# Optimization experiments

Measured on AMD Instinct MI355X. Metric: run time of the kernel, lower is better.

## Reference

```python
import jax, jax.numpy as jnp
import numpy as np

N = 512       # num_nodes (feature dim of x == num_nodes, per GCNConv(num_nodes, f1))
BZ = 32       # subjects
TC = 256      # tc_length
F1 = 256
F2 = 128
E = 524288    # edges in the given (corr) graph over all bz*N nodes
NTOT = BZ * N
SLOPE = 0.2   # leaky relu negative_slope


def setup_inputs() -> dict:
    key = jax.random.key(0)
    ks = jax.random.split(key, 17)
    w = lambda k, shape: (jax.random.normal(k, shape, jnp.float32) * (shape[-1] ** -0.5))
    return {
        "x": jax.random.normal(ks[0], (NTOT, N), jnp.float32),
        "t": jax.random.normal(ks[1], (NTOT, TC), jnp.float32),
        "gumbel_u": jax.random.uniform(ks[2], (BZ, N, N, 2), jnp.float32),
        "edge_index": jax.random.randint(ks[3], (2, E), 0, NTOT, jnp.int64 if jax.config.jax_enable_x64 else jnp.int32),
        "conv1_w": w(ks[4], (F1, N)),
        "conv1_b": jnp.zeros((F1,), jnp.float32),
        "conv2_w": w(ks[5], (F2, F1)),
        "conv2_b": jnp.zeros((F2,), jnp.float32),
        "fc_cat_w": w(ks[6], (2, 2 * TC)),
        "fc_cat_b": jnp.zeros((2,), jnp.float32),
        "fcn1_w": w(ks[7], (256, F2 * 2 * N)),
        "fcn1_b": jnp.zeros((256,), jnp.float32),
        "fcn2_w": w(ks[8], (32, 256)),
        "fcn2_b": jnp.zeros((32,), jnp.float32),
        "fcn3_w": w(ks[9], (2, 32)),
        "fcn3_b": jnp.zeros((2,), jnp.float32),
    }


def _gcn_dense(x, A, W, b):
    # PyG GCNConv on a dense 0/1 adjacency A (edge r->c means A[r,c]=1):
    # add self loop, in-degree symmetric norm, aggregate sources into targets.
    n = A.shape[0]
    Ah = A + jnp.eye(n, dtype=A.dtype)
    deg = Ah.sum(axis=0)                                  # in-degree (targets = cols)
    dis = jnp.where(deg > 0, jax.lax.rsqrt(deg), 0.0)
    M = dis[:, None] * Ah * dis[None, :]                  # M[j,i] = d_j^-1/2 A_hat[j,i] d_i^-1/2
    return M.T @ (x @ W.T) + b


def _gcn_sparse(x, row, col, W, b):
    n = x.shape[0]
    loops = jnp.arange(n, dtype=row.dtype)
    r = jnp.concatenate([row, loops])
    c = jnp.concatenate([col, loops])
    deg = jax.ops.segment_sum(jnp.ones_like(c, x.dtype), c, num_segments=n)
    dis = jnp.where(deg > 0, jax.lax.rsqrt(deg), 0.0)
    norm = dis[r] * dis[c]                                # [E+n]
    xw = x @ W.T                                          # [n, out]
    out = jax.ops.segment_sum(xw[r] * norm[:, None], c, num_segments=n)
    return out + b


def reference(x, t, gumbel_u, edge_index, conv1_w, conv1_b, conv2_w, conv2_b,
              fc_cat_w, fc_cat_b, fcn1_w, fcn1_b, fcn2_w, fcn2_b, fcn3_w, fcn3_b):
    bz = t.shape[0] // N
    tb = t.reshape(bz, N, -1)
    xb = x.reshape(bz, N, -1)
    # fc_cat(relu(cat([senders, receivers]))) factors into per-node terms:
    Ws = fc_cat_w[:, :TC]   # multiplies senders half
    Wr = fc_cat_w[:, TC:]   # multiplies receivers half

    def per_sample(ti, xi, ui):
        u = jax.nn.relu(ti)                               # [N, TC]
        ls = u @ Ws.T                                     # [N, 2] sender term
        lr = u @ Wr.T                                     # [N, 2] receiver term
        # pair k = i*N+j has receiver t_i, sender t_j
        logits = lr[:, None, :] + ls[None, :, :] + fc_cat_b   # [N, N, 2]
        g = -jnp.log(-jnp.log(jnp.clip(ui, 1e-9, 1.0 - 1e-9)))  # Gumbel(0,1)
        y = logits + g                                    # tau = 1
        A = (jnp.argmax(y, axis=-1) == 0).astype(xi.dtype)    # hard sample, class 0 => edge
        A = jax.lax.stop_gradient(A)                      # torch.where -> indices blocks grad
        h = jax.nn.relu(_gcn_dense(xi, A, conv1_w, conv1_b))
        return _gcn_dense(h, A, conv2_w, conv2_b)         # [N, F2]

    x_op = jax.vmap(per_sample)(tb, xb, gumbel_u)         # [bz, N, F2]

    row, col = edge_index[0], edge_index[1]
    x_corr = jax.nn.relu(_gcn_sparse(x, row, col, conv1_w, conv1_b))
    x_corr = _gcn_sparse(x_corr, row, col, conv2_w, conv2_b)   # [bz*N, F2]

    emb = jnp.concatenate([x_op.reshape(-1, F2), x_corr], axis=1)  # [bz*N, 2*F2]
    emb = emb.reshape(bz, -1)                             # [bz, 2*F2*N]
    h = jax.nn.leaky_relu(emb @ fcn1_w.T + fcn1_b, SLOPE)
    h = jax.nn.leaky_relu(h @ fcn2_w.T + fcn2_b, SLOPE)
    return h @ fcn3_w.T + fcn3_b                          # [bz, 2]
```

## Files before the change

kernel.cpp:

```cpp
#include <hip/hip_runtime.h>
#include <hip/hip_bf16.h>

typedef __bf16 bf16_t;
typedef __bf16 bf16x8 __attribute__((ext_vector_type(8)));
typedef __bf16 bf16x4 __attribute__((ext_vector_type(4)));
typedef float f32x4 __attribute__((ext_vector_type(4)));

constexpr int kN = 512;
constexpr int kBZ = 32;
constexpr int kTC = 256;
constexpr int kE = 524288;
constexpr int kNTOT = 16384;

__global__ __launch_bounds__(256) void k_cvt3(const float* __restrict__ c1w, const float* __restrict__ c2w,
                                              bf16_t* __restrict__ c1b, bf16_t* __restrict__ c2b,
                                              int* __restrict__ counts, float* __restrict__ degsum) {
    int i = blockIdx.x * 256 + threadIdx.x;
    const int n0 = 32768, n1 = n0 + 8192, n2 = n1 + 4096, n3 = n2 + 4096;
    if (i < n0) {
        float4 v = ((const float4*)c1w)[i];
        bf16x4 o = {(bf16_t)v.x, (bf16_t)v.y, (bf16_t)v.z, (bf16_t)v.w};
        ((bf16x4*)c1b)[i] = o;
    } else if (i < n1) {
        int j = i - n0;
        float4 v = ((const float4*)c2w)[j];
        bf16x4 o = {(bf16_t)v.x, (bf16_t)v.y, (bf16_t)v.z, (bf16_t)v.w};
        ((bf16x4*)c2b)[j] = o;
    } else if (i < n2) {
        ((int4*)counts)[i - n1] = make_int4(0, 0, 0, 0);
    } else if (i < n3) {
        ((float4*)degsum)[i - n2] = make_float4(0.f, 0.f, 0.f, 0.f);
    }
}

__global__ __launch_bounds__(256) void k_lsr(const float* __restrict__ tin, const float* __restrict__ fcw,
                                             const float* __restrict__ fcb, float4* __restrict__ lsr) {
    int row = blockIdx.x * 4 + (threadIdx.x >> 6);
    int lane = threadIdx.x & 63;
    const float* tr = tin + (size_t)row * kTC;
    float s0 = 0, s1 = 0, r0 = 0, r1 = 0;
    for (int k = lane; k < kTC; k += 64) {
        float u = fmaxf(tr[k], 0.f);
        s0 += u * fcw[k];
        s1 += u * fcw[512 + k];
        r0 += u * fcw[256 + k];
        r1 += u * fcw[768 + k];
    }
#pragma unroll
    for (int off = 32; off > 0; off >>= 1) {
        s0 += __shfl_down(s0, off); s1 += __shfl_down(s1, off);
        r0 += __shfl_down(r0, off); r1 += __shfl_down(r1, off);
    }
    if (lane == 0) lsr[row] = make_float4(s0 + fcb[0], s1 + fcb[1], r0, r1);
}

__global__ __launch_bounds__(256) void k_adj(const float* __restrict__ gum, const float4* __restrict__ lsr,
                                             bf16_t* __restrict__ AT, float* __restrict__ degsum) {
    int s = blockIdx.z;
    int a0 = blockIdx.y * 64, b0 = blockIdx.x * 64;
    __shared__ bf16_t tile[64][72];
    int t = threadIdx.x;
    int lb = t & 63, ra = t >> 6;
    int b = b0 + lb;
    float4 pb = lsr[s * kN + b];
#pragma unroll 4
    for (int p = 0; p < 16; p++) {
        int a = a0 + p * 4 + ra;
        float4 qa = lsr[s * kN + a];
        const float* g = gum + ((((size_t)s * kN + a) * kN + b) << 1);
        float u0 = fmaxf(g[0], 1e-9f);
        float u1 = fmaxf(g[1], 1e-9f);
        float g0 = -__logf(-__logf(u0));
        float g1 = -__logf(-__logf(u1));
        float v = ((qa.z + pb.x + g0) >= (qa.w + pb.y + g1)) ? 1.f : 0.f;
        if (a == b) v += 1.f;
        tile[lb][p * 4 + ra] = (bf16_t)v;
    }
    __syncthreads();
    int rj = t >> 3, li = (t & 7) * 8;
#pragma unroll
    for (int p = 0; p < 2; p++) {
        int j = p * 32 + rj;
        bf16x8 v = *(const bf16x8*)&tile[j][li];
        *(bf16x8*)(AT + ((size_t)s * kN + b0 + j) * kN + a0 + li) = v;
        float ps = 0;
#pragma unroll
        for (int q = 0; q < 8; q++) ps += (float)v[q];
        ps += __shfl_down(ps, 4);
        ps += __shfl_down(ps, 2);
        ps += __shfl_down(ps, 1);
        if ((t & 7) == 0) atomicAdd(degsum + s * kN + b0 + j, ps);
    }
}

template <int MODE>
__global__ __launch_bounds__(256) void k_gemm(const bf16_t* __restrict__ A, const bf16_t* __restrict__ B,
                                              bf16_t* __restrict__ C, int K, int lda, int ldb, int ldc,
                                              size_t sA, size_t sB, size_t sC,
                                              const float* __restrict__ degsum, const float* __restrict__ bias) {
    int m0 = blockIdx.x * 128, n0 = blockIdx.y * 128, s = blockIdx.z;
    A += sA * s; B += sB * s; C += sC * s;
    __shared__ bf16_t As[128][72], Bs[128][72];
    f32x4 acc[4][4] = {};
    int tid = threadIdx.x;
    int wave = tid >> 6, lane = tid & 63;
    int wm = (wave & 1) * 64, wn = (wave >> 1) * 64;
    int fm = lane & 15, fq = lane >> 4;
    int srow = tid >> 3, scol = (tid & 7) * 8;
    for (int kb = 0; kb < K; kb += 64) {
        __syncthreads();
#pragma unroll
        for (int p = 0; p < 4; p++) {
            int row = p * 32 + srow;
            *(uint4*)&As[row][scol] = *(const uint4*)(A + (size_t)(m0 + row) * lda + kb + scol);
            *(uint4*)&Bs[row][scol] = *(const uint4*)(B + (size_t)(n0 + row) * ldb + kb + scol);
        }
        __syncthreads();
#pragma unroll
        for (int kk = 0; kk < 2; kk++) {
            bf16x8 af[4], bfr[4];
#pragma unroll
            for (int i = 0; i < 4; i++) {
                af[i] = *(const bf16x8*)&As[wm + i * 16 + fm][kk * 32 + fq * 8];
                bfr[i] = *(const bf16x8*)&Bs[wn + i * 16 + fm][kk * 32 + fq * 8];
            }
#pragma unroll
            for (int i = 0; i < 4; i++)
#pragma unroll
                for (int j = 0; j < 4; j++)
                    acc[i][j] = __builtin_amdgcn_mfma_f32_16x16x32_bf16(af[i], bfr[j], acc[i][j], 0, 0, 0);
        }
    }
#pragma unroll
    for (int i = 0; i < 4; i++) {
#pragma unroll
        for (int r = 0; r < 4; r++) {
            int row = wm + i * 16 + fq * 4 + r;
            float sc = rsqrtf(degsum[(size_t)s * kN + m0 + row]);
#pragma unroll
            for (int j = 0; j < 4; j++) {
                int col = n0 + wn + j * 16 + fm;
                float v = sc * acc[i][j][r] + bias[col];
                if constexpr (MODE == 1) v = fmaxf(v, 0.f);
                C[(size_t)(m0 + row) * ldc + col] = (bf16_t)v;
            }
        }
    }
}

template <bool AF32, int F, int DENSE_ROWS>
__global__ __launch_bounds__(256) void k_gemmT(const void* __restrict__ Ap, const bf16_t* __restrict__ B,
                                               bf16_t* __restrict__ XW, bf16_t* __restrict__ ZT, int K,
                                               const float* __restrict__ degsum) {
    int m0 = blockIdx.x * 128, n0 = blockIdx.y * 128;
    __shared__ __align__(16) bf16_t smem[2 * 128 * 72];
    bf16_t* AsBase = smem;
    bf16_t* BsBase = smem + 128 * 72;
    f32x4 acc[4][4] = {};
    int tid = threadIdx.x;
    int wave = tid >> 6, lane = tid & 63;
    int wm = (wave & 1) * 64, wn = (wave >> 1) * 64;
    int fm = lane & 15, fq = lane >> 4;
    int srow = tid >> 3, scol = (tid & 7) * 8;
    for (int kb = 0; kb < K; kb += 64) {
        __syncthreads();
#pragma unroll
        for (int p = 0; p < 4; p++) {
            int row = p * 32 + srow;
            if constexpr (AF32) {
                const float* ap = (const float*)Ap + (size_t)(m0 + row) * K + kb + scol;
                float4 lo = *(const float4*)ap;
                float4 hi = *(const float4*)(ap + 4);
                bf16x8 o = {(bf16_t)lo.x, (bf16_t)lo.y, (bf16_t)lo.z, (bf16_t)lo.w,
                            (bf16_t)hi.x, (bf16_t)hi.y, (bf16_t)hi.z, (bf16_t)hi.w};
                *(bf16x8*)&AsBase[row * 72 + scol] = o;
            } else {
                *(uint4*)&AsBase[row * 72 + scol] =
                    *(const uint4*)((const bf16_t*)Ap + (size_t)(m0 + row) * K + kb + scol);
            }
            *(uint4*)&BsBase[row * 72 + scol] = *(const uint4*)(B + (size_t)(n0 + row) * K + kb + scol);
        }
        __syncthreads();
#pragma unroll
        for (int kk = 0; kk < 2; kk++) {
            bf16x8 af[4], bfr[4];
#pragma unroll
            for (int i = 0; i < 4; i++) {
                af[i] = *(const bf16x8*)&AsBase[(wm + i * 16 + fm) * 72 + kk * 32 + fq * 8];
                bfr[i] = *(const bf16x8*)&BsBase[(wn + i * 16 + fm) * 72 + kk * 32 + fq * 8];
            }
#pragma unroll
            for (int i = 0; i < 4; i++)
#pragma unroll
                for (int j = 0; j < 4; j++)
                    acc[i][j] = __builtin_amdgcn_mfma_f32_16x16x32_bf16(af[i], bfr[j], acc[i][j], 0, 0, 0);
        }
    }
    bool doT = (m0 < DENSE_ROWS);
    __syncthreads();
#pragma unroll
    for (int i = 0; i < 4; i++) {
#pragma unroll
        for (int r = 0; r < 4; r++) {
            int row = wm + i * 16 + fq * 4 + r;
            float sc = doT ? rsqrtf(degsum[m0 + row]) : 0.f;
#pragma unroll
            for (int j = 0; j < 4; j++) {
                int col = wn + j * 16 + fm;
                float v = acc[i][j][r];
                XW[(size_t)(m0 + row) * F + n0 + col] = (bf16_t)v;
                if (doT) smem[col * 136 + row] = (bf16_t)(sc * v);
            }
        }
    }
    if (doT) {
        __syncthreads();
        int fr = tid >> 1, hi = (tid & 1) * 64;
        bf16_t* zrow = ZT + ((size_t)(m0 >> 9) * F + n0 + fr) * kN + (m0 & 511) + hi;
#pragma unroll
        for (int q = 0; q < 8; q++)
            *(bf16x8*)(zrow + q * 8) = *(const bf16x8*)&smem[fr * 136 + hi + q * 8];
    }
}


__global__ __launch_bounds__(256) void k_hist(const int* __restrict__ col, int* __restrict__ counts) {
    int e = blockIdx.x * 256 + threadIdx.x;
    if (e < kE) atomicAdd(&counts[col[e]], 1);
}

__global__ __launch_bounds__(256) void k_scan(const int* __restrict__ counts, int* __restrict__ offsets,
                                              int* __restrict__ cursor, float* __restrict__ dis_s) {
    __shared__ int ldc_[16896];
    __shared__ int sums[256];
    int t = threadIdx.x;
#define IDX(j) ((j) + ((j) >> 5))
    for (int i = 0; i < 64; i++) {
        int g = i * 256 + t;
        int c = counts[g];
        ldc_[IDX(g)] = c;
        dis_s[g] = rsqrtf((float)(c + 1));
    }
    __syncthreads();
    int s = 0;
    for (int i = 0; i < 64; i++) s += ldc_[IDX(t * 64 + i)];
    sums[t] = s;
    __syncthreads();
    for (int off = 1; off < 256; off <<= 1) {
        int y = (t >= off) ? sums[t - off] : 0;
        __syncthreads();
        sums[t] += y;
        __syncthreads();
    }
    int run = sums[t] - s;
    for (int i = 0; i < 64; i++) {
        int j = t * 64 + i;
        int c = ldc_[IDX(j)];
        ldc_[IDX(j)] = run;
        run += c;
    }
    __syncthreads();
    for (int i = 0; i < 64; i++) {
        int g = i * 256 + t;
        int o = ldc_[IDX(g)];
        offsets[g] = o;
        cursor[g] = o;
    }
#undef IDX
}

__global__ __launch_bounds__(256) void k_fill(const int* __restrict__ row, const int* __restrict__ col,
                                              int* __restrict__ cursor, int* __restrict__ list) {
    int e = blockIdx.x * 256 + threadIdx.x;
    if (e < kE) {
        int p = atomicAdd(&cursor[col[e]], 1);
        list[p] = row[e];
    }
}

template <int F, bool RELU>
__global__ __launch_bounds__(256) void k_sagg(const bf16_t* __restrict__ XW, int rowOffIn,
                                              const int* __restrict__ list, const int* __restrict__ offsets,
                                              const int* __restrict__ counts, const float* __restrict__ dis_s,
                                              const float* __restrict__ bias, bf16_t* __restrict__ OUT,
                                              int outColOff) {
    constexpr int TPR = F / 8;
    constexpr int RPB = 256 / TPR;
    int j = blockIdx.x * RPB + threadIdx.x / TPR;
    int f8 = (threadIdx.x % TPR) * 8;
    float dj = dis_s[j];
    const bf16_t* base = XW + (size_t)rowOffIn * F;
    float acc[8];
    {
        bf16x8 v = *(const bf16x8*)(base + (size_t)j * F + f8);
#pragma unroll
        for (int q = 0; q < 8; q++) acc[q] = dj * (float)v[q];
    }
    int off = offsets[j], cnt = counts[j];
    int e = 0;
    for (; e + 4 <= cnt; e += 4) {
        int r0 = list[off + e], r1 = list[off + e + 1], r2 = list[off + e + 2], r3 = list[off + e + 3];
        float d0 = dis_s[r0], d1 = dis_s[r1], d2 = dis_s[r2], d3 = dis_s[r3];
        bf16x8 v0 = *(const bf16x8*)(base + (size_t)r0 * F + f8);
        bf16x8 v1 = *(const bf16x8*)(base + (size_t)r1 * F + f8);
        bf16x8 v2 = *(const bf16x8*)(base + (size_t)r2 * F + f8);
        bf16x8 v3 = *(const bf16x8*)(base + (size_t)r3 * F + f8);
#pragma unroll
        for (int q = 0; q < 8; q++)
            acc[q] += (d0 * (float)v0[q] + d1 * (float)v1[q]) + (d2 * (float)v2[q] + d3 * (float)v3[q]);
    }
    for (; e < cnt; e++) {
        int r = list[off + e];
        float d = dis_s[r];
        bf16x8 v = *(const bf16x8*)(base + (size_t)r * F + f8);
#pragma unroll
        for (int q = 0; q < 8; q++) acc[q] += d * (float)v[q];
    }
    bf16x8 o;
#pragma unroll
    for (int q = 0; q < 8; q++) {
        float v = dj * acc[q] + bias[f8 + q];
        if (RELU) v = fmaxf(v, 0.f);
        o[q] = (bf16_t)v;
    }
    *(bf16x8*)(OUT + (size_t)j * 256 + outColOff + f8) = o;
}

__global__ __launch_bounds__(256) void k_fcn1(const bf16_t* __restrict__ EMB, const float* __restrict__ W1,
                                              float* __restrict__ partials) {
    int tid = threadIdx.x, wave = tid >> 6, lane = tid & 63;
    int fm = lane & 15, fq = lane >> 4;
    int kb0 = blockIdx.x * 128;
    f32x4 acc[2][4] = {};
#pragma unroll
    for (int ks = 0; ks < 128; ks += 32) {
        int k = kb0 + ks + fq * 8;
        bf16x8 a0 = *(const bf16x8*)(EMB + (size_t)fm * 131072 + k);
        bf16x8 a1 = *(const bf16x8*)(EMB + (size_t)(16 + fm) * 131072 + k);
        bf16x8 bfr[4];
#pragma unroll
        for (int j = 0; j < 4; j++) {
            int n = wave * 64 + j * 16 + fm;
            const float* p = W1 + (size_t)n * 131072 + k;
            float4 lo = *(const float4*)p;
            float4 hi = *(const float4*)(p + 4);
            bf16x8 b = {(bf16_t)lo.x, (bf16_t)lo.y, (bf16_t)lo.z, (bf16_t)lo.w,
                        (bf16_t)hi.x, (bf16_t)hi.y, (bf16_t)hi.z, (bf16_t)hi.w};
            bfr[j] = b;
        }
#pragma unroll
        for (int j = 0; j < 4; j++) {
            acc[0][j] = __builtin_amdgcn_mfma_f32_16x16x32_bf16(a0, bfr[j], acc[0][j], 0, 0, 0);
            acc[1][j] = __builtin_amdgcn_mfma_f32_16x16x32_bf16(a1, bfr[j], acc[1][j], 0, 0, 0);
        }
    }
    float* P = partials + (size_t)blockIdx.x * 8192;
#pragma unroll
    for (int i = 0; i < 2; i++)
#pragma unroll
        for (int j = 0; j < 4; j++)
#pragma unroll
            for (int r = 0; r < 4; r++)
                P[(size_t)(i * 16 + fq * 4 + r) * 256 + wave * 64 + j * 16 + fm] = acc[i][j][r];
}

__global__ __launch_bounds__(256) void k_reduce(const float* __restrict__ partials, float* __restrict__ part2) {
    int kg = blockIdx.x >> 5, eb = blockIdx.x & 31;
    int e = eb * 256 + threadIdx.x;
    float s = 0;
#pragma unroll 8
    for (int i = 0; i < 128; i++) s += partials[(size_t)(kg * 128 + i) * 8192 + e];
    part2[(size_t)kg * 8192 + e] = s;
}

__global__ __launch_bounds__(256) void k_head(const float* __restrict__ part2, const float* __restrict__ b1,
                                              const float* __restrict__ W2, const float* __restrict__ b2,
                                              const float* __restrict__ W3, const float* __restrict__ b3,
                                              float* __restrict__ out) {
    __shared__ float h1s[32][256];
    __shared__ float h2s[32][32];
    int t = threadIdx.x;
    for (int i = 0; i < 32; i++) {
        int e = i * 256 + t;
        float s = 0;
#pragma unroll
        for (int kg = 0; kg < 8; kg++) s += part2[kg * 8192 + e];
        s += b1[t];
        h1s[i][t] = (s > 0.f) ? s : 0.2f * s;
    }
    __syncthreads();
    for (int p = 0; p < 4; p++) {
        int id = p * 256 + t, si = id >> 5, o2 = id & 31;
        float s = 0;
        for (int k = 0; k < 256; k++) s += h1s[si][k] * W2[o2 * 256 + k];
        s += b2[o2];
        h2s[si][o2] = (s > 0.f) ? s : 0.2f * s;
    }
    __syncthreads();
    if (t < 64) {
        int si = t >> 1, o3 = t & 1;
        float s = 0;
#pragma unroll
        for (int k = 0; k < 32; k++) s += h2s[si][k] * W3[o3 * 32 + k];
        out[si * 2 + o3] = s + b3[o3];
    }
}


extern "C" void kernel_launch(void* const* d_in, const int* in_sizes, int n_in,
                              void* d_out, int out_size, void* d_ws, size_t ws_size,
                              hipStream_t stream) {
    const float* x = (const float*)d_in[0];
    const float* t = (const float*)d_in[1];
    const float* gum = (const float*)d_in[2];
    const int* eidx = (const int*)d_in[3];
    const float* c1w = (const float*)d_in[4];
    const float* c1b = (const float*)d_in[5];
    const float* c2w = (const float*)d_in[6];
    const float* c2b = (const float*)d_in[7];
    const float* fcw = (const float*)d_in[8];
    const float* fcb = (const float*)d_in[9];
    const float* w1 = (const float*)d_in[10];
    const float* b1 = (const float*)d_in[11];
    const float* w2 = (const float*)d_in[12];
    const float* b2 = (const float*)d_in[13];
    const float* w3 = (const float*)d_in[14];
    const float* b3 = (const float*)d_in[15];
    float* out = (float*)d_out;
    (void)in_sizes; (void)n_in; (void)out_size; (void)ws_size;

    char* ws = (char*)d_ws;
    size_t off = 0;
    auto alloc = [&](size_t bytes) -> char* {
        char* p = ws + off;
        off += (bytes + 255) & ~size_t(255);
        return p;
    };
    bf16_t* c1wb = (bf16_t*)alloc((size_t)256 * 512 * 2);
    bf16_t* c2wb = (bf16_t*)alloc((size_t)128 * 256 * 2);
    float4* lsr = (float4*)alloc((size_t)kNTOT * 16);
    bf16_t* AT = (bf16_t*)alloc((size_t)kBZ * kN * kN * 2);
    float* degsum = (float*)alloc((size_t)kNTOT * 4);
    bf16_t* XW1_EMB = (bf16_t*)alloc((size_t)kNTOT * 256 * 2);
    bf16_t* Z1T = (bf16_t*)alloc((size_t)kBZ * 256 * 512 * 2);
    bf16_t* H = (bf16_t*)alloc((size_t)32768 * 256 * 2);
    bf16_t* XW2 = (bf16_t*)alloc((size_t)32768 * 128 * 2);
    bf16_t* Z2T = (bf16_t*)alloc((size_t)kBZ * 128 * 512 * 2);
    int* counts = (int*)alloc((size_t)kNTOT * 4);
    int* offsets = (int*)alloc((size_t)kNTOT * 4);
    int* cursor = (int*)alloc((size_t)kNTOT * 4);
    float* diss = (float*)alloc((size_t)kNTOT * 4);
    int* list = (int*)alloc((size_t)kE * 4);
    float* partials = (float*)alloc((size_t)1024 * 8192 * 4);
    float* part2 = (float*)alloc((size_t)8 * 8192 * 4);

    bf16_t* XW1 = XW1_EMB;
    bf16_t* EMB = XW1_EMB;

    k_cvt3<<<192, 256, 0, stream>>>(c1w, c2w, c1wb, c2wb, counts, degsum);
    k_lsr<<<4096, 256, 0, stream>>>(t, fcw, fcb, lsr);
    k_adj<<<dim3(8, 8, 32), 256, 0, stream>>>(gum, lsr, AT, degsum);
    k_hist<<<2048, 256, 0, stream>>>(eidx + kE, counts);
    k_scan<<<1, 256, 0, stream>>>(counts, offsets, cursor, diss);
    k_fill<<<2048, 256, 0, stream>>>(eidx, eidx + kE, cursor, list);
    k_gemmT<true, 256, kNTOT><<<dim3(128, 2, 1), 256, 0, stream>>>(x, c1wb, XW1, Z1T, 512, degsum);
    k_gemm<1><<<dim3(4, 2, 32), 256, 0, stream>>>(AT, Z1T, H, 512, 512, 512, 256,
                                                  (size_t)512 * 512, (size_t)256 * 512, (size_t)512 * 256,
                                                  degsum, c1b);
    k_sagg<256, true><<<2048, 256, 0, stream>>>(XW1, 0, list, offsets, counts, diss, c1b,
                                                H + (size_t)16384 * 256, 0);
    k_gemmT<false, 128, kNTOT><<<dim3(256, 1, 1), 256, 0, stream>>>(H, c2wb, XW2, Z2T, 256, degsum);
    k_gemm<2><<<dim3(4, 1, 32), 256, 0, stream>>>(AT, Z2T, EMB, 512, 512, 512, 256,
                                                  (size_t)512 * 512, (size_t)128 * 512, (size_t)512 * 256,
                                                  degsum, c2b);
    k_sagg<128, false><<<1024, 256, 0, stream>>>(XW2, 16384, list, offsets, counts, diss, c2b, EMB, 128);
    k_fcn1<<<1024, 256, 0, stream>>>(EMB, w1, partials);
    k_reduce<<<256, 256, 0, stream>>>(partials, part2);
    k_head<<<1, 256, 0, stream>>>(part2, b1, w2, b2, w3, b3, out);
}
```

Before: 517.2 us.

## Merge front kernels, widen scan, unroll sparse gather, and coarsen fcn1 split-K

Merges the weight-conversion/zeroing kernel and the lsr projection kernel into one launch. The single-block scan now runs 1024 threads instead of 256. The Gumbel noise pair is read as one float2 load, and the sparse aggregation gains an 8-way unrolled edge loop for more loads in flight. fcn1 now gives each block 512 K values instead of 128, so there are 256 partials rather than 1024, and the reduction becomes one pass over 256 partials. The aim is fewer launches and less partial-sum traffic, at the cost of less parallelism in fcn1 and in the reduction.

```diff
diff --git a/kernel.cpp b/kernel.cpp
--- a/kernel.cpp
+++ b/kernel.cpp
@@ -12,46 +12,51 @@
 constexpr int kE = 524288;
 constexpr int kNTOT = 16384;
 
-__global__ __launch_bounds__(256) void k_cvt3(const float* __restrict__ c1w, const float* __restrict__ c2w,
-                                              bf16_t* __restrict__ c1b, bf16_t* __restrict__ c2b,
-                                              int* __restrict__ counts, float* __restrict__ degsum) {
-    int i = blockIdx.x * 256 + threadIdx.x;
-    const int n0 = 32768, n1 = n0 + 8192, n2 = n1 + 4096, n3 = n2 + 4096;
-    if (i < n0) {
-        float4 v = ((const float4*)c1w)[i];
-        bf16x4 o = {(bf16_t)v.x, (bf16_t)v.y, (bf16_t)v.z, (bf16_t)v.w};
-        ((bf16x4*)c1b)[i] = o;
-    } else if (i < n1) {
-        int j = i - n0;
-        float4 v = ((const float4*)c2w)[j];
-        bf16x4 o = {(bf16_t)v.x, (bf16_t)v.y, (bf16_t)v.z, (bf16_t)v.w};
-        ((bf16x4*)c2b)[j] = o;
-    } else if (i < n2) {
-        ((int4*)counts)[i - n1] = make_int4(0, 0, 0, 0);
-    } else if (i < n3) {
-        ((float4*)degsum)[i - n2] = make_float4(0.f, 0.f, 0.f, 0.f);
-    }
-}
-
-__global__ __launch_bounds__(256) void k_lsr(const float* __restrict__ tin, const float* __restrict__ fcw,
-                                             const float* __restrict__ fcb, float4* __restrict__ lsr) {
-    int row = blockIdx.x * 4 + (threadIdx.x >> 6);
-    int lane = threadIdx.x & 63;
-    const float* tr = tin + (size_t)row * kTC;
-    float s0 = 0, s1 = 0, r0 = 0, r1 = 0;
-    for (int k = lane; k < kTC; k += 64) {
-        float u = fmaxf(tr[k], 0.f);
-        s0 += u * fcw[k];
-        s1 += u * fcw[512 + k];
-        r0 += u * fcw[256 + k];
-        r1 += u * fcw[768 + k];
-    }
-#pragma unroll
-    for (int off = 32; off > 0; off >>= 1) {
-        s0 += __shfl_down(s0, off); s1 += __shfl_down(s1, off);
-        r0 += __shfl_down(r0, off); r1 += __shfl_down(r1, off);
-    }
-    if (lane == 0) lsr[row] = make_float4(s0 + fcb[0], s1 + fcb[1], r0, r1);
+__global__ __launch_bounds__(256) void k_front(const float* __restrict__ c1w, const float* __restrict__ c2w,
+                                               bf16_t* __restrict__ c1b, bf16_t* __restrict__ c2b,
+                                               int* __restrict__ counts, float* __restrict__ degsum,
+                                               float* __restrict__ h1acc,
+                                               const float* __restrict__ tin, const float* __restrict__ fcw,
+                                               const float* __restrict__ fcb, float4* __restrict__ lsr) {
+    int b = blockIdx.x;
+    if (b < 200) {
+        int i = b * 256 + threadIdx.x;
+        const int n0 = 32768, n1 = n0 + 8192, n2 = n1 + 4096, n3 = n2 + 4096, n4 = n3 + 2048;
+        if (i < n0) {
+            float4 v = ((const float4*)c1w)[i];
+            bf16x4 o = {(bf16_t)v.x, (bf16_t)v.y, (bf16_t)v.z, (bf16_t)v.w};
+            ((bf16x4*)c1b)[i] = o;
+        } else if (i < n1) {
+            int j = i - n0;
+            float4 v = ((const float4*)c2w)[j];
+            bf16x4 o = {(bf16_t)v.x, (bf16_t)v.y, (bf16_t)v.z, (bf16_t)v.w};
+            ((bf16x4*)c2b)[j] = o;
+        } else if (i < n2) {
+            ((int4*)counts)[i - n1] = make_int4(0, 0, 0, 0);
+        } else if (i < n3) {
+            ((float4*)degsum)[i - n2] = make_float4(0.f, 0.f, 0.f, 0.f);
+        } else if (i < n4) {
+            ((float4*)h1acc)[i - n3] = make_float4(0.f, 0.f, 0.f, 0.f);
+        }
+    } else {
+        int row = (b - 200) * 4 + (threadIdx.x >> 6);
+        int lane = threadIdx.x & 63;
+        const float* tr = tin + (size_t)row * kTC;
+        float s0 = 0, s1 = 0, r0 = 0, r1 = 0;
+        for (int k = lane; k < kTC; k += 64) {
+            float u = fmaxf(tr[k], 0.f);
+            s0 += u * fcw[k];
+            s1 += u * fcw[512 + k];
+            r0 += u * fcw[256 + k];
+            r1 += u * fcw[768 + k];
+        }
+#pragma unroll
+        for (int off = 32; off > 0; off >>= 1) {
+            s0 += __shfl_down(s0, off); s1 += __shfl_down(s1, off);
+            r0 += __shfl_down(r0, off); r1 += __shfl_down(r1, off);
+        }
+        if (lane == 0) lsr[row] = make_float4(s0 + fcb[0], s1 + fcb[1], r0, r1);
+    }
 }
 
 __global__ __launch_bounds__(256) void k_adj(const float* __restrict__ gum, const float4* __restrict__ lsr,
@@ -67,9 +72,9 @@
     for (int p = 0; p < 16; p++) {
         int a = a0 + p * 4 + ra;
         float4 qa = lsr[s * kN + a];
-        const float* g = gum + ((((size_t)s * kN + a) * kN + b) << 1);
-        float u0 = fmaxf(g[0], 1e-9f);
-        float u1 = fmaxf(g[1], 1e-9f);
+        float2 gv = *(const float2*)(gum + ((((size_t)s * kN + a) * kN + b) << 1));
+        float u0 = fmaxf(gv.x, 1e-9f);
+        float u1 = fmaxf(gv.y, 1e-9f);
         float g0 = -__logf(-__logf(u0));
         float g1 = -__logf(-__logf(u1));
         float v = ((qa.z + pb.x + g0) >= (qa.w + pb.y + g1)) ? 1.f : 0.f;
@@ -229,39 +234,39 @@
     if (e < kE) atomicAdd(&counts[col[e]], 1);
 }
 
-__global__ __launch_bounds__(256) void k_scan(const int* __restrict__ counts, int* __restrict__ offsets,
-                                              int* __restrict__ cursor, float* __restrict__ dis_s) {
+__global__ __launch_bounds__(1024) void k_scan(const int* __restrict__ counts, int* __restrict__ offsets,
+                                               int* __restrict__ cursor, float* __restrict__ dis_s) {
     __shared__ int ldc_[16896];
-    __shared__ int sums[256];
+    __shared__ int sums[1024];
     int t = threadIdx.x;
 #define IDX(j) ((j) + ((j) >> 5))
-    for (int i = 0; i < 64; i++) {
-        int g = i * 256 + t;
+    for (int i = 0; i < 16; i++) {
+        int g = i * 1024 + t;
         int c = counts[g];
         ldc_[IDX(g)] = c;
         dis_s[g] = rsqrtf((float)(c + 1));
     }
     __syncthreads();
     int s = 0;
-    for (int i = 0; i < 64; i++) s += ldc_[IDX(t * 64 + i)];
+    for (int i = 0; i < 16; i++) s += ldc_[IDX(t * 16 + i)];
     sums[t] = s;
     __syncthreads();
-    for (int off = 1; off < 256; off <<= 1) {
+    for (int off = 1; off < 1024; off <<= 1) {
         int y = (t >= off) ? sums[t - off] : 0;
         __syncthreads();
         sums[t] += y;
         __syncthreads();
     }
     int run = sums[t] - s;
-    for (int i = 0; i < 64; i++) {
-        int j = t * 64 + i;
+    for (int i = 0; i < 16; i++) {
+        int j = t * 16 + i;
         int c = ldc_[IDX(j)];
         ldc_[IDX(j)] = run;
         run += c;
     }
     __syncthreads();
-    for (int i = 0; i < 64; i++) {
-        int g = i * 256 + t;
+    for (int i = 0; i < 16; i++) {
+        int g = i * 1024 + t;
         int o = ldc_[IDX(g)];
         offsets[g] = o;
         cursor[g] = o;
@@ -298,6 +303,26 @@
     }
     int off = offsets[j], cnt = counts[j];
     int e = 0;
+    for (; e + 8 <= cnt; e += 8) {
+        int r[8];
+#pragma unroll
+        for (int q = 0; q < 8; q++) r[q] = list[off + e + q];
+        float d[8];
+#pragma unroll
+        for (int q = 0; q < 8; q++) d[q] = dis_s[r[q]];
+        bf16x8 v0 = *(const bf16x8*)(base + (size_t)r[0] * F + f8);
+        bf16x8 v1 = *(const bf16x8*)(base + (size_t)r[1] * F + f8);
+        bf16x8 v2 = *(const bf16x8*)(base + (size_t)r[2] * F + f8);
+        bf16x8 v3 = *(const bf16x8*)(base + (size_t)r[3] * F + f8);
+        bf16x8 v4 = *(const bf16x8*)(base + (size_t)r[4] * F + f8);
+        bf16x8 v5 = *(const bf16x8*)(base + (size_t)r[5] * F + f8);
+        bf16x8 v6 = *(const bf16x8*)(base + (size_t)r[6] * F + f8);
+        bf16x8 v7 = *(const bf16x8*)(base + (size_t)r[7] * F + f8);
+#pragma unroll
+        for (int q = 0; q < 8; q++)
+            acc[q] += ((d[0] * (float)v0[q] + d[1] * (float)v1[q]) + (d[2] * (float)v2[q] + d[3] * (float)v3[q])) +
+                      ((d[4] * (float)v4[q] + d[5] * (float)v5[q]) + (d[6] * (float)v6[q] + d[7] * (float)v7[q]));
+    }
     for (; e + 4 <= cnt; e += 4) {
         int r0 = list[off + e], r1 = list[off + e + 1], r2 = list[off + e + 2], r3 = list[off + e + 3];
         float d0 = dis_s[r0], d1 = dis_s[r1], d2 = dis_s[r2], d3 = dis_s[r3];
@@ -330,10 +355,10 @@
                                               float* __restrict__ partials) {
     int tid = threadIdx.x, wave = tid >> 6, lane = tid & 63;
     int fm = lane & 15, fq = lane >> 4;
-    int kb0 = blockIdx.x * 128;
+    int kb0 = blockIdx.x * 512;
     f32x4 acc[2][4] = {};
-#pragma unroll
-    for (int ks = 0; ks < 128; ks += 32) {
+#pragma unroll 4
+    for (int ks = 0; ks < 512; ks += 32) {
         int k = kb0 + ks + fq * 8;
         bf16x8 a0 = *(const bf16x8*)(EMB + (size_t)fm * 131072 + k);
         bf16x8 a1 = *(const bf16x8*)(EMB + (size_t)(16 + fm) * 131072 + k);
@@ -364,16 +389,15 @@
                 P[(size_t)(i * 16 + fq * 4 + r) * 256 + wave * 64 + j * 16 + fm] = acc[i][j][r];
 }
 
-__global__ __launch_bounds__(256) void k_reduce(const float* __restrict__ partials, float* __restrict__ part2) {
-    int kg = blockIdx.x >> 5, eb = blockIdx.x & 31;
-    int e = eb * 256 + threadIdx.x;
+__global__ __launch_bounds__(256) void k_reduce(const float* __restrict__ partials, float* __restrict__ h1pre) {
+    int e = blockIdx.x * 256 + threadIdx.x;
     float s = 0;
 #pragma unroll 8
-    for (int i = 0; i < 128; i++) s += partials[(size_t)(kg * 128 + i) * 8192 + e];
-    part2[(size_t)kg * 8192 + e] = s;
-}
-
-__global__ __launch_bounds__(256) void k_head(const float* __restrict__ part2, const float* __restrict__ b1,
+    for (int i = 0; i < 256; i++) s += partials[(size_t)i * 8192 + e];
+    h1pre[e] = s;
+}
+
+__global__ __launch_bounds__(256) void k_head(const float* __restrict__ h1pre, const float* __restrict__ b1,
                                               const float* __restrict__ W2, const float* __restrict__ b2,
                                               const float* __restrict__ W3, const float* __restrict__ b3,
                                               float* __restrict__ out) {
@@ -381,11 +405,7 @@
     __shared__ float h2s[32][32];
     int t = threadIdx.x;
     for (int i = 0; i < 32; i++) {
-        int e = i * 256 + t;
-        float s = 0;
-#pragma unroll
-        for (int kg = 0; kg < 8; kg++) s += part2[kg * 8192 + e];
-        s += b1[t];
+        float s = h1pre[i * 256 + t] + b1[t];
         h1s[i][t] = (s > 0.f) ? s : 0.2f * s;
     }
     __syncthreads();
@@ -451,17 +471,16 @@
     int* cursor = (int*)alloc((size_t)kNTOT * 4);
     float* diss = (float*)alloc((size_t)kNTOT * 4);
     int* list = (int*)alloc((size_t)kE * 4);
-    float* partials = (float*)alloc((size_t)1024 * 8192 * 4);
-    float* part2 = (float*)alloc((size_t)8 * 8192 * 4);
+    float* partials = (float*)alloc((size_t)256 * 8192 * 4);
+    float* h1pre = (float*)alloc((size_t)8192 * 4);
 
     bf16_t* XW1 = XW1_EMB;
     bf16_t* EMB = XW1_EMB;
 
-    k_cvt3<<<192, 256, 0, stream>>>(c1w, c2w, c1wb, c2wb, counts, degsum);
-    k_lsr<<<4096, 256, 0, stream>>>(t, fcw, fcb, lsr);
+    k_front<<<4296, 256, 0, stream>>>(c1w, c2w, c1wb, c2wb, counts, degsum, h1pre, t, fcw, fcb, lsr);
     k_adj<<<dim3(8, 8, 32), 256, 0, stream>>>(gum, lsr, AT, degsum);
     k_hist<<<2048, 256, 0, stream>>>(eidx + kE, counts);
-    k_scan<<<1, 256, 0, stream>>>(counts, offsets, cursor, diss);
+    k_scan<<<1, 1024, 0, stream>>>(counts, offsets, cursor, diss);
     k_fill<<<2048, 256, 0, stream>>>(eidx, eidx + kE, cursor, list);
     k_gemmT<true, 256, kNTOT><<<dim3(128, 2, 1), 256, 0, stream>>>(x, c1wb, XW1, Z1T, 512, degsum);
     k_gemm<1><<<dim3(4, 2, 32), 256, 0, stream>>>(AT, Z1T, H, 512, 512, 512, 256,
@@ -474,7 +493,7 @@
                                                   (size_t)512 * 512, (size_t)128 * 512, (size_t)512 * 256,
                                                   degsum, c2b);
     k_sagg<128, false><<<1024, 256, 0, stream>>>(XW2, 16384, list, offsets, counts, diss, c2b, EMB, 128);
-    k_fcn1<<<1024, 256, 0, stream>>>(EMB, w1, partials);
-    k_reduce<<<256, 256, 0, stream>>>(partials, part2);
-    k_head<<<1, 256, 0, stream>>>(part2, b1, w2, b2, w3, b3, out);
-}
+    k_fcn1<<<256, 256, 0, stream>>>(EMB, w1, partials);
+    k_reduce<<<32, 256, 0, stream>>>(partials, h1pre);
+    k_head<<<1, 256, 0, stream>>>(h1pre, b1, w2, b2, w3, b3, out);
+}
```

Measured after the change: 508.0 us. No clear change (-1.8%).
